# Kernel optimization log

Measured on AMD Instinct MI355X. Metric: run time of the kernel, lower is better.

The kernel has to match this reference:

```python
import jax, jax.numpy as jnp
import numpy as np

COMMITMENT_COST = 0.25


def setup_inputs() -> dict:
    key = jax.random.key(0)
    k1, k2 = jax.random.split(key)
    z = jax.random.normal(k1, (64, 256, 32, 32), dtype=jnp.float32)
    # codebook init ~ U(-1/K, 1/K) as in torch module
    K, D = 1024, 256
    emb = jax.random.uniform(k2, (K, D), dtype=jnp.float32, minval=-1.0 / K, maxval=1.0 / K)
    return {"z": z, "emb": emb}


def reference(z, emb):
    # b c h w -> b h w c
    zt = jnp.transpose(z, (0, 2, 3, 1))
    B, H, W, C = zt.shape
    zf = zt.reshape(-1, C)  # (b*h*w, c)
    # squared euclidean distances: ||z||^2 + ||e||^2 - 2 z.e
    d = (jnp.sum(zf * zf, axis=1, keepdims=True)
         + jnp.sum(emb * emb, axis=1)
         - 2.0 * jnp.einsum('nd,kd->nk', zf, emb))
    min_encoding_indices = jnp.argmin(d, axis=1)  # (b*h*w,)
    z_quantized = emb[min_encoding_indices].reshape(B, H, W, C)
    commitment_loss = COMMITMENT_COST * jnp.mean((jax.lax.stop_gradient(z_quantized) - zt) ** 2)
    codebook_loss = jnp.mean((z_quantized - jax.lax.stop_gradient(zt)) ** 2)
    loss = commitment_loss + codebook_loss
    # straight-through estimator
    z_quantized = zt + jax.lax.stop_gradient(z_quantized - zt)
    out = jnp.transpose(z_quantized, (0, 3, 1, 2))  # b c h w
    return out, loss, min_encoding_indices.reshape(B, H, W)
```

## Files before the change

### kernel.cpp

```cpp
#include <hip/hip_runtime.h>
#include <math.h>

#define KCODES 1024
#define DDIM   256
#define HWSZ   1024
#define CHW    262144
#define LOSS_OFF 16777216
#define IDX_OFF  16777217
#define TAU_GAP  1.4e-4f
#define RR4      4

#define WS_ZH   0u
#define WS_EH   33554432u
#define WS_EL   34078720u
#define WS_AN   34603008u
#define WS_BN   34865152u
#define WS_LIST 34869248u
#define WS_CNT  35131392u
#define WS_NEED 35131396u

#define OB_ZH   0
#define OB_EH   8388608
#define OB_EL   8519680
#define OB_AN   8650752
#define OB_BN   8716288
#define OB_LIST 8717312
#define OB_CNT  8782848

typedef __attribute__((ext_vector_type(8))) short short8v;
typedef __attribute__((ext_vector_type(4))) float float4v;

#define GLOAD_LDS(gsrc, ldst)                                                   \
    __builtin_amdgcn_global_load_lds(                                           \
        (const __attribute__((address_space(1))) void*)(gsrc),                  \
        (__attribute__((address_space(3))) void*)(ldst), 16, 0, 0)

static __device__ __forceinline__ unsigned short bf16_rne(float f) {
    unsigned u = __float_as_uint(f);
    return (unsigned short)((u + 0x7FFFu + ((u >> 16) & 1u)) >> 16);
}
static __device__ __forceinline__ float bf16_tf(unsigned short h) {
    return __uint_as_float(((unsigned)h) << 16);
}

__global__ __launch_bounds__(64) void vq_prep_bn(const float* __restrict__ emb,
                                                 float* __restrict__ Bn,
                                                 float* __restrict__ loss_slot,
                                                 int* __restrict__ cnt) {
    int k = blockIdx.x * 64 + threadIdx.x;
    if (k == 0) { *cnt = 0; loss_slot[0] = 0.f; }
    if (k >= KCODES) return;
    const float* e = emb + (size_t)k * DDIM;
    float half[2];
    #pragma unroll
    for (int h = 0; h < 2; ++h) {
        const float* q = e + (h << 7);
        float r[8];
        #pragma unroll
        for (int j = 0; j < 8; ++j) r[j] = __fmul_rn(q[j], q[j]);
        for (int i = 8; i < 128; i += 8) {
            #pragma unroll
            for (int j = 0; j < 8; ++j)
                r[j] = __fadd_rn(r[j], __fmul_rn(q[i + j], q[i + j]));
        }
        half[h] = __fadd_rn(
            __fadd_rn(__fadd_rn(r[0], r[1]), __fadd_rn(r[2], r[3])),
            __fadd_rn(__fadd_rn(r[4], r[5]), __fadd_rn(r[6], r[7])));
    }
    Bn[k] = __fadd_rn(half[0], half[1]);
}

__global__ __launch_bounds__(256) void vq_prep_scatter(const float* __restrict__ emb,
                                                       unsigned short* __restrict__ EHg,
                                                       unsigned short* __restrict__ ELg) {
    int task = blockIdx.x * 256 + threadIdx.x;
    int k  = task >> 5;
    int dg = task & 31;
    const float* e = emb + (size_t)k * DDIM + (dg << 3);
    float4 v0 = *(const float4*)e;
    float4 v1 = *(const float4*)(e + 4);
    float f[8] = {v0.x, v0.y, v0.z, v0.w, v1.x, v1.y, v1.z, v1.w};
    short8v hv, lv;
    #pragma unroll
    for (int j = 0; j < 8; ++j) {
        unsigned short hb = bf16_rne(f[j]);
        unsigned short lb = bf16_rne(f[j] - bf16_tf(hb));
        hv[j] = (short)hb; lv[j] = (short)lb;
    }
    int base = ((k >> 4) << 12) + ((dg >> 2) << 9) + (((k & 15) + ((dg & 3) << 4)) << 3);
    *(short8v*)(EHg + base) = hv;
    *(short8v*)(ELg + base) = lv;
}

__global__ __launch_bounds__(256) void vq_zprep2(const float* __restrict__ z,
                                                 unsigned short* __restrict__ ZHg,
                                                 float* __restrict__ An) {
    __shared__ float hs[2][128];
    const int t = threadIdx.x;
    const int nb = blockIdx.x;
    const int b = nb >> 3, hw0 = (nb & 7) << 7;
    const int h = t >> 7, n = t & 127;
    const float* src = z + (size_t)b * CHW + (size_t)(h << 7) * HWSZ + hw0 + n;
    unsigned short* zbase = ZHg + (size_t)nb * 32768 + ((n >> 4) << 9) + ((n & 15) << 3);
    float r[8];
    #pragma unroll
    for (int blk8 = 0; blk8 < 16; ++blk8) {
        float f[8];
        #pragma unroll
        for (int j = 0; j < 8; ++j) f[j] = src[(size_t)((blk8 << 3) + j) * HWSZ];
        if (blk8 == 0) {
            #pragma unroll
            for (int j = 0; j < 8; ++j) r[j] = __fmul_rn(f[j], f[j]);
        } else {
            #pragma unroll
            for (int j = 0; j < 8; ++j) r[j] = __fadd_rn(r[j], __fmul_rn(f[j], f[j]));
        }
        short8v hv;
        #pragma unroll
        for (int j = 0; j < 8; ++j) hv[j] = (short)bf16_rne(f[j]);
        int d = (h << 7) + (blk8 << 3);
        int s32 = d >> 5, g = (d >> 3) & 3;
        *(short8v*)(zbase + s32 * 4096 + (g << 7)) = hv;
    }
    hs[h][n] = __fadd_rn(
        __fadd_rn(__fadd_rn(r[0], r[1]), __fadd_rn(r[2], r[3])),
        __fadd_rn(__fadd_rn(r[4], r[5]), __fadd_rn(r[6], r[7])));
    __syncthreads();
    if (t < 128) An[nb * 128 + t] = __fadd_rn(hs[0][t], hs[1][t]);
}

template<bool WRITE_OUT>
__global__ __launch_bounds__(512, 4) void vq_argmin2g(
        const unsigned short* __restrict__ ZHg,
        const unsigned short* __restrict__ EHg, const unsigned short* __restrict__ ELg,
        const float* __restrict__ An, const float* __restrict__ Bn,
        float* __restrict__ idx_out, int* __restrict__ list, int* __restrict__ cnt,
        float* __restrict__ loss_slot, float* __restrict__ outp,
        const float* __restrict__ emb) {
    __shared__ uint4 ZH4[512];
    __shared__ uint4 EBUF4[2048];
    __shared__ float BNs[1024];
    unsigned short* ZH = (unsigned short*)ZH4;
    unsigned short* EH = (unsigned short*)EBUF4;
    unsigned short* EL = EH + 8192;

    const int t = threadIdx.x;
    const int bid = blockIdx.x;
    const int nb = ((bid & 7) << 6) + (bid >> 3);
    const int b   = nb >> 3;
    const int hw0 = (nb & 7) << 7;
    const int lane = t & 63, w = t >> 6;
    const int kwv = w >> 1, nwv = w & 1;
    const int l8 = lane << 3, g2 = lane >> 4;

    BNs[t] = Bn[t];
    BNs[t + 512] = Bn[t + 512];

    float an[4];
    #pragma unroll
    for (int nf = 0; nf < 4; ++nf)
        an[nf] = An[nb * 128 + nwv * 64 + nf * 16 + (lane & 15)];

    float mv1[4], mv2[4]; int mi1[4];
    #pragma unroll
    for (int i = 0; i < 4; ++i) { mv1[i] = 3.4e38f; mv2[i] = 3.4e38f; mi1[i] = 0x7fffffff; }

    const uint4* zh4 = (const uint4*)ZHg + (size_t)nb * 4096;
    const uint4* eh4 = (const uint4*)EHg;
    const uint4* el4 = (const uint4*)ELg;

    for (int kt = 0; kt < 4; ++kt) {
        float4v acc[4][4];
        #pragma unroll
        for (int a = 0; a < 4; ++a)
            #pragma unroll
            for (int c = 0; c < 4; ++c) acc[a][c] = (float4v){0.f, 0.f, 0.f, 0.f};

        for (int s32 = 0; s32 < 8; ++s32) {
            __syncthreads();
            GLOAD_LDS(zh4 + s32 * 512 + t, &ZH4[t]);
            #pragma unroll
            for (int p = 0; p < 4; ++p) {
                int s = p * 512 + t;
                int arr = s >> 10, ss = s & 1023;
                const uint4* src = (arr ? el4 : eh4)
                    + (size_t)(((kt << 4) + (ss >> 6)) << 9) + (s32 << 6) + (ss & 63);
                uint4* dst = (arr ? ((uint4*)EL) : ((uint4*)EH)) + ss;
                GLOAD_LDS(src, dst);
            }
            __syncthreads();
            short8v ah[4], al[4], bh[4];
            #pragma unroll
            for (int kf = 0; kf < 4; ++kf) {
                int base = ((kwv * 4 + kf) << 9) + l8;
                ah[kf] = *(const short8v*)&EH[base];
                al[kf] = *(const short8v*)&EL[base];
            }
            #pragma unroll
            for (int nf = 0; nf < 4; ++nf)
                bh[nf] = *(const short8v*)&ZH[((nwv * 4 + nf) << 9) + l8];
            #pragma unroll
            for (int kf = 0; kf < 4; ++kf)
                #pragma unroll
                for (int nf = 0; nf < 4; ++nf) {
                    acc[kf][nf] = __builtin_amdgcn_mfma_f32_16x16x32_bf16(ah[kf], bh[nf], acc[kf][nf], 0, 0, 0);
                    acc[kf][nf] = __builtin_amdgcn_mfma_f32_16x16x32_bf16(al[kf], bh[nf], acc[kf][nf], 0, 0, 0);
                }
        }
        #pragma unroll
        for (int kf = 0; kf < 4; ++kf)
            #pragma unroll
            for (int nf = 0; nf < 4; ++nf)
                #pragma unroll
                for (int r = 0; r < 4; ++r) {
                    int k = kt * 256 + kwv * 64 + kf * 16 + g2 * 4 + r;
                    float s = __fsub_rn(__fadd_rn(an[nf], BNs[k]),
                                        __fmul_rn(2.0f, acc[kf][nf][r]));
                    if (s < mv1[nf] || (s == mv1[nf] && k < mi1[nf])) {
                        mv2[nf] = fminf(mv2[nf], mv1[nf]);
                        mv1[nf] = s; mi1[nf] = k;
                    } else if (s < mv2[nf]) mv2[nf] = s;
                }
    }

    __syncthreads();
    float* REDv = (float*)EBUF4;
    int*   REDi = (int*)((char*)EBUF4 + 8192);
    float* REDw = (float*)((char*)EBUF4 + 16384);
    int*   FIDX = (int*)((char*)EBUF4 + 24576);

    #pragma unroll
    for (int nf = 0; nf < 4; ++nf) {
        int nl = nf * 16 + (lane & 15);
        int slot = kwv * 4 + g2;
        REDv[(nwv * 64 + nl) * 16 + slot] = mv1[nf];
        REDi[(nwv * 64 + nl) * 16 + slot] = mi1[nf];
        REDw[(nwv * 64 + nl) * 16 + slot] = mv2[nf];
    }
    __syncthreads();
    if (t < 128) {
        float bv = 3.4e38f, b2 = 3.4e38f; int bi = 0x7fffffff;
        #pragma unroll
        for (int s = 0; s < 16; ++s) {
            float v1 = REDv[t * 16 + s];
            float v2 = REDw[t * 16 + s];
            int   i1 = REDi[t * 16 + s];
            if (v1 < bv || (v1 == bv && i1 < bi)) { b2 = fminf(b2, bv); bv = v1; bi = i1; }
            else b2 = fminf(b2, v1);
            b2 = fminf(b2, v2);
        }
        int n_glob = nb * 128 + t;
        idx_out[n_glob] = (float)bi;
        FIDX[t] = bi;
        if (b2 - bv < TAU_GAP) {
            int pos = atomicAdd(cnt, 1);
            list[pos] = n_glob;
        }
        float lsum = bv;
        #pragma unroll
        for (int off = 32; off > 0; off >>= 1)
            lsum += __shfl_down(lsum, off, 64);
        if ((t & 63) == 0) atomicAdd(loss_slot, lsum * (1.25f / 16777216.f));
    }
    if (WRITE_OUT) {
        __syncthreads();
        int n_loc = t & 127, cg = t >> 7;
        int idx = FIDX[n_loc];
        int hw = hw0 + n_loc;
        const float4* erow = (const float4*)(emb + (size_t)idx * DDIM + (cg << 6));
        float* obase = outp + (size_t)b * CHW + (size_t)(cg << 6) * HWSZ + hw;
        #pragma unroll 4
        for (int q = 0; q < 16; ++q) {
            float4 v = erow[q];
            obase[(size_t)(q * 4 + 0) * HWSZ] = v.x;
            obase[(size_t)(q * 4 + 1) * HWSZ] = v.y;
            obase[(size_t)(q * 4 + 2) * HWSZ] = v.z;
            obase[(size_t)(q * 4 + 3) * HWSZ] = v.w;
        }
    }
}

template<bool WRITE_OUT>
__global__ __launch_bounds__(512) void vq_rescore_r(
        const float* __restrict__ z, const float* __restrict__ emb,
        const float* __restrict__ An, const float* __restrict__ Bn,
        float* __restrict__ idx_out, const int* __restrict__ list,
        const int* __restrict__ cnt, float* __restrict__ outp) {
    const int c = *cnt;
    const int t = threadIdx.x;
    const int lane = t & 63, w = t >> 6;
    const int g  = lane >> 4;
    const int ch = lane & 15;
    __shared__ float zs[RR4][256];
    __shared__ float Ars[RR4];
    __shared__ int   rid[RR4];
    __shared__ float wsv[RR4][8];
    __shared__ int   wsi[RR4][8];
    __shared__ int   wbi[RR4];

    for (int base = blockIdx.x * RR4; base < c; base += gridDim.x * RR4) {
        const int nrows = min(RR4, c - base);
        __syncthreads();
        if (t < nrows) { int n = list[base + t]; rid[t] = n; Ars[t] = An[n]; }
        __syncthreads();
        for (int i = t; i < (nrows << 8); i += 512) {
            int r = i >> 8, d = i & 255;
            int n = rid[r];
            zs[r][d] = z[(size_t)(n >> 10) * CHW + (size_t)d * HWSZ + (n & 1023)];
        }
        __syncthreads();

        float4 zr[RR4][4];
        #pragma unroll
        for (int r = 0; r < RR4; ++r)
            #pragma unroll
            for (int it = 0; it < 4; ++it)
                zr[r][it] = *(const float4*)&zs[r][(it * 16 + ch) << 2];

        float bv[RR4]; int bi[RR4];
        #pragma unroll
        for (int r = 0; r < RR4; ++r) { bv[r] = 3.4e38f; bi[r] = 0x7fffffff; }

        for (int p = 0; p < 32; ++p) {
            int cc = p * 32 + w * 4 + g;
            const float4* e4 = (const float4*)(emb + (size_t)cc * DDIM);
            double part[RR4];
            #pragma unroll
            for (int r = 0; r < RR4; ++r) part[r] = 0.0;
            #pragma unroll
            for (int it = 0; it < 4; ++it) {
                float4 ev = e4[it * 16 + ch];
                #pragma unroll
                for (int r = 0; r < RR4; ++r) {
                    float4 zv = zr[r][it];
                    part[r] += (double)ev.x * zv.x + (double)ev.y * zv.y
                             + (double)ev.z * zv.z + (double)ev.w * zv.w;
                }
            }
            #pragma unroll
            for (int off = 1; off <= 8; off <<= 1)
                #pragma unroll
                for (int r = 0; r < RR4; ++r)
                    part[r] += __shfl_xor(part[r], off, 64);
            float Bk = Bn[cc];
            #pragma unroll
            for (int r = 0; r < RR4; ++r) {
                float s = __fsub_rn(__fadd_rn(Ars[r], Bk),
                                    __fmul_rn(2.0f, (float)part[r]));
                if (s < bv[r]) { bv[r] = s; bi[r] = cc; }
            }
        }
        #pragma unroll
        for (int r = 0; r < RR4; ++r) {
            float v = bv[r]; int i1 = bi[r];
            #pragma unroll
            for (int off = 16; off <= 32; off <<= 1) {
                float ov = __shfl_xor(v, off, 64);
                int   oi = __shfl_xor(i1, off, 64);
                if (ov < v || (ov == v && oi < i1)) { v = ov; i1 = oi; }
            }
            if (lane == 0) { wsv[r][w] = v; wsi[r][w] = i1; }
        }
        __syncthreads();
        if (t < nrows) {
            float v = wsv[t][0]; int i1 = wsi[t][0];
            #pragma unroll
            for (int j = 1; j < 8; ++j) {
                float ov = wsv[t][j]; int oi = wsi[t][j];
                if (ov < v || (ov == v && oi < i1)) { v = ov; i1 = oi; }
            }
            idx_out[rid[t]] = (float)i1;
            wbi[t] = i1;
        }
        if (WRITE_OUT) {
            __syncthreads();
            for (int i = t; i < (nrows << 8); i += 512) {
                int r = i >> 8, d = i & 255;
                int n = rid[r];
                outp[(size_t)(n >> 10) * CHW + (size_t)d * HWSZ + (n & 1023)]
                    = emb[(size_t)wbi[r] * DDIM + d];
            }
        }
    }
}

__global__ __launch_bounds__(256) void vq_epilogue(const float* __restrict__ emb,
                                                   float* __restrict__ outp,
                                                   const float* __restrict__ idxf) {
    const int t  = threadIdx.x;
    const int nc = blockIdx.x;
    const int b  = nc >> 4;
    const int hw = ((nc & 15) << 6) + (t & 63);
    const int n  = (b << 10) + hw;
    const int idx = (int)idxf[n];
    const float* erow = emb + (size_t)idx * DDIM;
    const size_t zb = (size_t)b * CHW + hw;

    const int cbase = (t >> 6) << 2;
    #pragma unroll 4
    for (int cq = 0; cq < 16; ++cq) {
        int c = cbase + (cq << 4);
        float4 q4 = *reinterpret_cast<const float4*>(erow + c);
        outp[zb + (size_t)(c + 0) * HWSZ] = q4.x;
        outp[zb + (size_t)(c + 1) * HWSZ] = q4.y;
        outp[zb + (size_t)(c + 2) * HWSZ] = q4.z;
        outp[zb + (size_t)(c + 3) * HWSZ] = q4.w;
    }
}

extern "C" void kernel_launch(void* const* d_in, const int* in_sizes, int n_in,
                              void* d_out, int out_size, void* d_ws, size_t ws_size,
                              hipStream_t stream) {
    const float* z   = (const float*)d_in[0];
    const float* emb = (const float*)d_in[1];
    float* out       = (float*)d_out;
    float* loss_slot = out + LOSS_OFF;
    float* idx_out   = out + IDX_OFF;

    if (ws_size >= (size_t)WS_NEED) {
        char* ws = (char*)d_ws;
        unsigned short* ZHg = (unsigned short*)(ws + WS_ZH);
        unsigned short* EHg = (unsigned short*)(ws + WS_EH);
        unsigned short* ELg = (unsigned short*)(ws + WS_EL);
        float* An = (float*)(ws + WS_AN);
        float* Bn = (float*)(ws + WS_BN);
        int*  list = (int*)(ws + WS_LIST);
        int*  cnt  = (int*)(ws + WS_CNT);

        vq_prep_bn          <<<dim3(16),   dim3(64),  0, stream>>>(emb, Bn, loss_slot, cnt);
        vq_prep_scatter     <<<dim3(128),  dim3(256), 0, stream>>>(emb, EHg, ELg);
        vq_zprep2           <<<dim3(512),  dim3(256), 0, stream>>>(z, ZHg, An);
        vq_argmin2g<true>   <<<dim3(512),  dim3(512), 0, stream>>>(ZHg, EHg, ELg, An, Bn,
                                 idx_out, list, cnt, loss_slot, out, emb);
        vq_rescore_r<true>  <<<dim3(2048), dim3(512), 0, stream>>>(z, emb, An, Bn,
                                 idx_out, list, cnt, out);
    } else {
        unsigned short* ZHg = (unsigned short*)(out + OB_ZH);
        unsigned short* EHg = (unsigned short*)(out + OB_EH);
        unsigned short* ELg = (unsigned short*)(out + OB_EL);
        float* An = out + OB_AN;
        float* Bn = out + OB_BN;
        int*  list = (int*)(out + OB_LIST);
        int*  cnt  = (int*)(out + OB_CNT);

        vq_prep_bn          <<<dim3(16),   dim3(64),  0, stream>>>(emb, Bn, loss_slot, cnt);
        vq_prep_scatter     <<<dim3(128),  dim3(256), 0, stream>>>(emb, EHg, ELg);
        vq_zprep2           <<<dim3(512),  dim3(256), 0, stream>>>(z, ZHg, An);
        vq_argmin2g<false>  <<<dim3(512),  dim3(512), 0, stream>>>(ZHg, EHg, ELg, An, Bn,
                                 idx_out, list, cnt, loss_slot, out, emb);
        vq_rescore_r<false> <<<dim3(2048), dim3(512), 0, stream>>>(z, emb, An, Bn,
                                 idx_out, list, cnt, out);
        vq_epilogue         <<<dim3(1024), dim3(256), 0, stream>>>(emb, out, idx_out);
    }
}
```

Before: 220.2 us.

## Retile argmin to 64-row blocks and rescore from a transposed z copy

```diff
diff --git a/kernel.cpp b/kernel.cpp
--- a/kernel.cpp
+++ b/kernel.cpp
@@ -18,6 +18,8 @@
 #define WS_LIST 34869248u
 #define WS_CNT  35131392u
 #define WS_NEED 35131396u
+#define WS_ZT   35131648u
+#define WS_NEED2 102240512u
 
 #define OB_ZH   0
 #define OB_EH   8388608
@@ -94,7 +96,8 @@
 
 __global__ __launch_bounds__(256) void vq_zprep2(const float* __restrict__ z,
                                                  unsigned short* __restrict__ ZHg,
-                                                 float* __restrict__ An) {
+                                                 float* __restrict__ An,
+                                                 float* __restrict__ zT) {
     __shared__ float hs[2][128];
     const int t = threadIdx.x;
     const int nb = blockIdx.x;
@@ -102,6 +105,7 @@
     const int h = t >> 7, n = t & 127;
     const float* src = z + (size_t)b * CHW + (size_t)(h << 7) * HWSZ + hw0 + n;
     unsigned short* zbase = ZHg + (size_t)nb * 32768 + ((n >> 4) << 9) + ((n & 15) << 3);
+    float* ztb = zT ? (zT + ((size_t)nb * 128 + n) * DDIM + (h << 7)) : nullptr;
     float r[8];
     #pragma unroll
     for (int blk8 = 0; blk8 < 16; ++blk8) {
@@ -121,6 +125,10 @@
         int d = (h << 7) + (blk8 << 3);
         int s32 = d >> 5, g = (d >> 3) & 3;
         *(short8v*)(zbase + s32 * 4096 + (g << 7)) = hv;
+        if (ztb) {
+            *(float4*)(ztb + (blk8 << 3))     = make_float4(f[0], f[1], f[2], f[3]);
+            *(float4*)(ztb + (blk8 << 3) + 4) = make_float4(f[4], f[5], f[6], f[7]);
+        }
     }
     hs[h][n] = __fadd_rn(
         __fadd_rn(__fadd_rn(r[0], r[1]), __fadd_rn(r[2], r[3])),
@@ -130,42 +138,42 @@
 }
 
 template<bool WRITE_OUT>
-__global__ __launch_bounds__(512, 4) void vq_argmin2g(
+__global__ __launch_bounds__(256, 4) void vq_argmin4b(
         const unsigned short* __restrict__ ZHg,
         const unsigned short* __restrict__ EHg, const unsigned short* __restrict__ ELg,
         const float* __restrict__ An, const float* __restrict__ Bn,
         float* __restrict__ idx_out, int* __restrict__ list, int* __restrict__ cnt,
         float* __restrict__ loss_slot, float* __restrict__ outp,
         const float* __restrict__ emb) {
-    __shared__ uint4 ZH4[512];
+    __shared__ uint4 ZCH4[256];
     __shared__ uint4 EBUF4[2048];
     __shared__ float BNs[1024];
-    unsigned short* ZH = (unsigned short*)ZH4;
+    unsigned short* ZCH = (unsigned short*)ZCH4;
     unsigned short* EH = (unsigned short*)EBUF4;
     unsigned short* EL = EH + 8192;
 
     const int t = threadIdx.x;
     const int bid = blockIdx.x;
-    const int nb = ((bid & 7) << 6) + (bid >> 3);
-    const int b   = nb >> 3;
-    const int hw0 = (nb & 7) << 7;
+    const int nb = ((bid & 7) << 7) + (bid >> 3);
+    const int b   = nb >> 4;
+    const int hw0 = (nb & 15) << 6;
     const int lane = t & 63, w = t >> 6;
-    const int kwv = w >> 1, nwv = w & 1;
+    const int kwv = w;
     const int l8 = lane << 3, g2 = lane >> 4;
 
-    BNs[t] = Bn[t];
-    BNs[t + 512] = Bn[t + 512];
+    #pragma unroll
+    for (int p = 0; p < 4; ++p) BNs[p * 256 + t] = Bn[p * 256 + t];
 
     float an[4];
     #pragma unroll
     for (int nf = 0; nf < 4; ++nf)
-        an[nf] = An[nb * 128 + nwv * 64 + nf * 16 + (lane & 15)];
+        an[nf] = An[nb * 64 + nf * 16 + (lane & 15)];
 
     float mv1[4], mv2[4]; int mi1[4];
     #pragma unroll
     for (int i = 0; i < 4; ++i) { mv1[i] = 3.4e38f; mv2[i] = 3.4e38f; mi1[i] = 0x7fffffff; }
 
-    const uint4* zh4 = (const uint4*)ZHg + (size_t)nb * 4096;
+    const uint4* zh4 = (const uint4*)ZHg + (size_t)(nb >> 1) * 4096 + (nb & 1) * 256;
     const uint4* eh4 = (const uint4*)EHg;
     const uint4* el4 = (const uint4*)ELg;
 
@@ -178,10 +186,10 @@
 
         for (int s32 = 0; s32 < 8; ++s32) {
             __syncthreads();
-            GLOAD_LDS(zh4 + s32 * 512 + t, &ZH4[t]);
-            #pragma unroll
-            for (int p = 0; p < 4; ++p) {
-                int s = p * 512 + t;
+            GLOAD_LDS(zh4 + s32 * 512 + t, &ZCH4[t]);
+            #pragma unroll
+            for (int p = 0; p < 8; ++p) {
+                int s = p * 256 + t;
                 int arr = s >> 10, ss = s & 1023;
                 const uint4* src = (arr ? el4 : eh4)
                     + (size_t)(((kt << 4) + (ss >> 6)) << 9) + (s32 << 6) + (ss & 63);
@@ -198,7 +206,7 @@
             }
             #pragma unroll
             for (int nf = 0; nf < 4; ++nf)
-                bh[nf] = *(const short8v*)&ZH[((nwv * 4 + nf) << 9) + l8];
+                bh[nf] = *(const short8v*)&ZCH[(nf << 9) + l8];
             #pragma unroll
             for (int kf = 0; kf < 4; ++kf)
                 #pragma unroll
@@ -225,20 +233,20 @@
 
     __syncthreads();
     float* REDv = (float*)EBUF4;
-    int*   REDi = (int*)((char*)EBUF4 + 8192);
-    float* REDw = (float*)((char*)EBUF4 + 16384);
-    int*   FIDX = (int*)((char*)EBUF4 + 24576);
+    int*   REDi = (int*)((char*)EBUF4 + 4096);
+    float* REDw = (float*)((char*)EBUF4 + 8192);
+    int*   FIDX = (int*)((char*)EBUF4 + 12288);
 
     #pragma unroll
     for (int nf = 0; nf < 4; ++nf) {
         int nl = nf * 16 + (lane & 15);
         int slot = kwv * 4 + g2;
-        REDv[(nwv * 64 + nl) * 16 + slot] = mv1[nf];
-        REDi[(nwv * 64 + nl) * 16 + slot] = mi1[nf];
-        REDw[(nwv * 64 + nl) * 16 + slot] = mv2[nf];
+        REDv[nl * 16 + slot] = mv1[nf];
+        REDi[nl * 16 + slot] = mi1[nf];
+        REDw[nl * 16 + slot] = mv2[nf];
     }
     __syncthreads();
-    if (t < 128) {
+    if (t < 64) {
         float bv = 3.4e38f, b2 = 3.4e38f; int bi = 0x7fffffff;
         #pragma unroll
         for (int s = 0; s < 16; ++s) {
@@ -249,7 +257,7 @@
             else b2 = fminf(b2, v1);
             b2 = fminf(b2, v2);
         }
-        int n_glob = nb * 128 + t;
+        int n_glob = nb * 64 + t;
         idx_out[n_glob] = (float)bi;
         FIDX[t] = bi;
         if (b2 - bv < TAU_GAP) {
@@ -260,11 +268,11 @@
         #pragma unroll
         for (int off = 32; off > 0; off >>= 1)
             lsum += __shfl_down(lsum, off, 64);
-        if ((t & 63) == 0) atomicAdd(loss_slot, lsum * (1.25f / 16777216.f));
+        if (t == 0) atomicAdd(loss_slot, lsum * (1.25f / 16777216.f));
     }
     if (WRITE_OUT) {
         __syncthreads();
-        int n_loc = t & 127, cg = t >> 7;
+        int n_loc = t & 63, cg = t >> 6;
         int idx = FIDX[n_loc];
         int hw = hw0 + n_loc;
         const float4* erow = (const float4*)(emb + (size_t)idx * DDIM + (cg << 6));
@@ -281,8 +289,9 @@
 }
 
 template<bool WRITE_OUT>
-__global__ __launch_bounds__(512) void vq_rescore_r(
-        const float* __restrict__ z, const float* __restrict__ emb,
+__global__ __launch_bounds__(512) void vq_rescore_z(
+        const float* __restrict__ z, const float* __restrict__ zT,
+        const float* __restrict__ emb,
         const float* __restrict__ An, const float* __restrict__ Bn,
         float* __restrict__ idx_out, const int* __restrict__ list,
         const int* __restrict__ cnt, float* __restrict__ outp) {
@@ -303,10 +312,17 @@
         __syncthreads();
         if (t < nrows) { int n = list[base + t]; rid[t] = n; Ars[t] = An[n]; }
         __syncthreads();
-        for (int i = t; i < (nrows << 8); i += 512) {
-            int r = i >> 8, d = i & 255;
-            int n = rid[r];
-            zs[r][d] = z[(size_t)(n >> 10) * CHW + (size_t)d * HWSZ + (n & 1023)];
+        if (zT) {
+            for (int i = t; i < (nrows << 8); i += 512) {
+                int r = i >> 8, d = i & 255;
+                zs[r][d] = zT[(size_t)rid[r] * DDIM + d];
+            }
+        } else {
+            for (int i = t; i < (nrows << 8); i += 512) {
+                int r = i >> 8, d = i & 255;
+                int n = rid[r];
+                zs[r][d] = z[(size_t)(n >> 10) * CHW + (size_t)d * HWSZ + (n & 1023)];
+            }
         }
         __syncthreads();
 
@@ -427,13 +443,26 @@
         int*  list = (int*)(ws + WS_LIST);
         int*  cnt  = (int*)(ws + WS_CNT);
 
-        vq_prep_bn          <<<dim3(16),   dim3(64),  0, stream>>>(emb, Bn, loss_slot, cnt);
-        vq_prep_scatter     <<<dim3(128),  dim3(256), 0, stream>>>(emb, EHg, ELg);
-        vq_zprep2           <<<dim3(512),  dim3(256), 0, stream>>>(z, ZHg, An);
-        vq_argmin2g<true>   <<<dim3(512),  dim3(512), 0, stream>>>(ZHg, EHg, ELg, An, Bn,
-                                 idx_out, list, cnt, loss_slot, out, emb);
-        vq_rescore_r<true>  <<<dim3(2048), dim3(512), 0, stream>>>(z, emb, An, Bn,
-                                 idx_out, list, cnt, out);
+        if (ws_size >= (size_t)WS_NEED2) {
+            float* zT = (float*)(ws + WS_ZT);
+            vq_prep_bn         <<<dim3(16),   dim3(64),  0, stream>>>(emb, Bn, loss_slot, cnt);
+            vq_prep_scatter    <<<dim3(128),  dim3(256), 0, stream>>>(emb, EHg, ELg);
+            vq_zprep2          <<<dim3(512),  dim3(256), 0, stream>>>(z, ZHg, An, zT);
+            vq_argmin4b<true>  <<<dim3(1024), dim3(256), 0, stream>>>(ZHg, EHg, ELg, An, Bn,
+                                    idx_out, list, cnt, loss_slot, out, emb);
+            vq_rescore_z<true> <<<dim3(2048), dim3(512), 0, stream>>>(z, zT, emb, An, Bn,
+                                    idx_out, list, cnt, out);
+        } else {
+            float* zT = out;
+            vq_prep_bn          <<<dim3(16),   dim3(64),  0, stream>>>(emb, Bn, loss_slot, cnt);
+            vq_prep_scatter     <<<dim3(128),  dim3(256), 0, stream>>>(emb, EHg, ELg);
+            vq_zprep2           <<<dim3(512),  dim3(256), 0, stream>>>(z, ZHg, An, zT);
+            vq_argmin4b<false>  <<<dim3(1024), dim3(256), 0, stream>>>(ZHg, EHg, ELg, An, Bn,
+                                     idx_out, list, cnt, loss_slot, out, emb);
+            vq_rescore_z<false> <<<dim3(2048), dim3(512), 0, stream>>>(z, zT, emb, An, Bn,
+                                     idx_out, list, cnt, out);
+            vq_epilogue         <<<dim3(1024), dim3(256), 0, stream>>>(emb, out, idx_out);
+        }
     } else {
         unsigned short* ZHg = (unsigned short*)(out + OB_ZH);
         unsigned short* EHg = (unsigned short*)(out + OB_EH);
@@ -445,10 +474,10 @@
 
         vq_prep_bn          <<<dim3(16),   dim3(64),  0, stream>>>(emb, Bn, loss_slot, cnt);
         vq_prep_scatter     <<<dim3(128),  dim3(256), 0, stream>>>(emb, EHg, ELg);
-        vq_zprep2           <<<dim3(512),  dim3(256), 0, stream>>>(z, ZHg, An);
-        vq_argmin2g<false>  <<<dim3(512),  dim3(512), 0, stream>>>(ZHg, EHg, ELg, An, Bn,
+        vq_zprep2           <<<dim3(512),  dim3(256), 0, stream>>>(z, ZHg, An, nullptr);
+        vq_argmin4b<false>  <<<dim3(1024), dim3(256), 0, stream>>>(ZHg, EHg, ELg, An, Bn,
                                  idx_out, list, cnt, loss_slot, out, emb);
-        vq_rescore_r<false> <<<dim3(2048), dim3(512), 0, stream>>>(z, emb, An, Bn,
+        vq_rescore_z<false> <<<dim3(2048), dim3(512), 0, stream>>>(z, nullptr, emb, An, Bn,
                                  idx_out, list, cnt, out);
         vq_epilogue         <<<dim3(1024), dim3(256), 0, stream>>>(emb, out, idx_out);
     }
```

After: 298.4 us. +35.5%, slower.
